# Kernel optimization log

Hardware: AMD Instinct MI355X
Metric: run time of the kernel (lower is better)

The kernel has to match this reference:

```python
import jax, jax.numpy as jnp
import numpy as np

N, D = 4096, 768
TEMPERATURE = 0.05


def setup_inputs() -> dict:
    key = jax.random.key(0)
    k1, k2 = jax.random.split(key)
    scale = 1.0 / jnp.sqrt(jnp.float32(D))  # keep dot/T in exp's safe range
    anchors = jax.random.normal(k1, (N, D), dtype=jnp.float32) * scale
    positives = jax.random.normal(k2, (N, D), dtype=jnp.float32) * scale
    return {"anchors": anchors, "positives": positives}


def reference(anchors, positives):
    # logits[j, i] = dot(anchor_j, positive_i) / T  -- single matmul replaces
    # the O(N^2) python-loop torch.dot calls.
    logits = jnp.einsum("jd,id->ji", anchors, positives) / TEMPERATURE  # [N, N]
    e = jnp.exp(logits)
    # Original code: negative_sum starts at exp(dot(anchor_j, positive_j)/T)
    # (the diagonal) and then adds exp(dot(anchor_j, positive_i)/T) for ALL i
    # (so the own positive is counted twice).
    denom = jnp.diagonal(e) + e.sum(axis=1)  # [N]
    # Original bug: positive_similarity is overwritten inside the inner loop,
    # so the numerator is the similarity to the LAST positive (index N-1).
    log_num = logits[:, -1]  # [N]
    loss = -(log_num - jnp.log(denom))
    return loss.sum()
```

## Files before the change

### kernel.cpp

```cpp
#include <hip/hip_runtime.h>
#include <hip/hip_bf16.h>

#define N 4096
#define D 768
#define LN2 0.69314718055994530942f
#define QSCALE 5.371583f

typedef __attribute__((ext_vector_type(4))) int   i32x4;
typedef __attribute__((ext_vector_type(8))) int   i32x8;
typedef __attribute__((ext_vector_type(4))) float f32x4;

#define EXP2F(x) __builtin_amdgcn_exp2f(x)
#define LOG2F(x) __builtin_amdgcn_logf(x)

#define GLDS16(g, l) __builtin_amdgcn_global_load_lds( \
    (const __attribute__((address_space(1))) void*)(g), \
    (__attribute__((address_space(3))) void*)(l), 16, 0, 0)


__global__ void convert_kernel(const float* __restrict__ A, const float* __restrict__ B,
                               unsigned* __restrict__ Af8, unsigned* __restrict__ Bf8,
                               float* __restrict__ out) {
    if (blockIdx.x == 0 && threadIdx.x == 0) out[0] = 0.0f;
    const int total = N * D / 4;
    int idx = blockIdx.x * blockDim.x + threadIdx.x;
    int stride = gridDim.x * blockDim.x;
    for (int i = idx; i < total; i += stride) {
        float4 a = ((const float4*)A)[i];
        float4 b = ((const float4*)B)[i];
        int pa = __builtin_amdgcn_cvt_pk_fp8_f32(a.x * QSCALE, a.y * QSCALE, 0, 0);
        pa     = __builtin_amdgcn_cvt_pk_fp8_f32(a.z * QSCALE, a.w * QSCALE, pa, 1);
        int pb = __builtin_amdgcn_cvt_pk_fp8_f32(b.x * QSCALE, b.y * QSCALE, 0, 0);
        pb     = __builtin_amdgcn_cvt_pk_fp8_f32(b.z * QSCALE, b.w * QSCALE, pb, 1);
        Af8[i] = (unsigned)pa;
        Bf8[i] = (unsigned)pb;
    }
}

__global__ __launch_bounds__(256) void gemm_kernel(const unsigned char* __restrict__ Af8,
                                                   const unsigned char* __restrict__ Bf8,
                                                   float* __restrict__ partial,
                                                   float* __restrict__ diagS,
                                                   float* __restrict__ lastS) {
    __shared__ __align__(16) unsigned char As[128 * 128];
    __shared__ __align__(16) unsigned char Bs[128 * 128];
    __shared__ float rowsum2[2][128];

    const int t    = threadIdx.x;
    const int bid  = blockIdx.x;
    const int xcd  = bid & 7;
    const int ii   = bid >> 3;
    const int bRow = ((xcd >> 1) << 3) + (ii >> 4);
    const int bCol = ((xcd & 1) << 4) + (ii & 15);
    const int lane = t & 63;
    const int w    = t >> 6;
    const int wr   = w >> 1;
    const int wc   = w & 1;
    const int lr   = lane & 15;
    const int hi   = lane >> 4;

    const int srow = t >> 3;
    const int sc   = t & 7;
    const int gcv  = sc ^ (srow & 7);
    const size_t aOff = (size_t)(bRow * 128 + srow) * D + gcv * 16;
    const size_t bOff = (size_t)(bCol * 128 + srow) * D + gcv * 16;

    f32x4 acc[4][4] = {};
    const int NT = D / 128;

    union Frag { i32x8 v; i32x4 h[2]; };

#define LDFRAG(DST, ARRBUF, ROW) do {                                                   \
    (DST).h[0] = *(const i32x4*)&(ARRBUF)[(ROW) * 128 + ((hi ^ (lr & 7)) * 16)];        \
    (DST).h[1] = *(const i32x4*)&(ARRBUF)[(ROW) * 128 + (((hi + 4) ^ (lr & 7)) * 16)];  \
} while (0)

    for (int tt = 0; tt < NT; ++tt) {
        const size_t kb = (size_t)tt * 128;
        #pragma unroll
        for (int inst = 0; inst < 4; ++inst) {
            GLDS16(Af8 + aOff + (size_t)inst * 32 * D + kb, &As[inst * 4096 + w * 1024]);
            GLDS16(Bf8 + bOff + (size_t)inst * 32 * D + kb, &Bs[inst * 4096 + w * 1024]);
        }
        asm volatile("s_waitcnt vmcnt(0)" ::: "memory");
        __builtin_amdgcn_s_barrier();
        __builtin_amdgcn_sched_barrier(0);

        Frag bfr[4];
        #pragma unroll
        for (int nf = 0; nf < 4; ++nf)
            LDFRAG(bfr[nf], Bs, wc * 64 + nf * 16 + lr);
        __builtin_amdgcn_s_setprio(1);
        #pragma unroll
        for (int mf = 0; mf < 4; ++mf) {
            Frag a8;
            LDFRAG(a8, As, wr * 64 + mf * 16 + lr);
            #pragma unroll
            for (int nf = 0; nf < 4; ++nf)
                acc[mf][nf] = __builtin_amdgcn_mfma_scale_f32_16x16x128_f8f6f4(
                    a8.v, bfr[nf].v, acc[mf][nf], 0, 0, 0, 0x7F7F7F7F, 0, 0x7F7F7F7F);
        }
        __builtin_amdgcn_s_setprio(0);
        asm volatile("s_waitcnt lgkmcnt(0)" ::: "memory");
        __builtin_amdgcn_sched_barrier(0);
        __builtin_amdgcn_s_barrier();
        __builtin_amdgcn_sched_barrier(0);
    }
#undef LDFRAG

    const int rifb = hi * 4;

    if (bRow == bCol && wr == wc) {
        #pragma unroll
        for (int mf = 0; mf < 4; ++mf)
            #pragma unroll
            for (int reg = 0; reg < 4; ++reg)
                if (lr == rifb + reg)
                    diagS[bRow * 128 + wr * 64 + mf * 16 + rifb + reg] = acc[mf][mf][reg];
    }

    if (bCol == (N / 128 - 1) && wc == 1 && lr == 15) {
        #pragma unroll
        for (int mf = 0; mf < 4; ++mf)
            #pragma unroll
            for (int reg = 0; reg < 4; ++reg)
                lastS[bRow * 128 + wr * 64 + mf * 16 + rifb + reg] = acc[mf][3][reg];
    }

    #pragma unroll
    for (int mf = 0; mf < 4; ++mf) {
        #pragma unroll
        for (int reg = 0; reg < 4; ++reg) {
            float s = EXP2F(acc[mf][0][reg]) + EXP2F(acc[mf][1][reg]) +
                      EXP2F(acc[mf][2][reg]) + EXP2F(acc[mf][3][reg]);
            s += __shfl_xor(s, 1);
            s += __shfl_xor(s, 2);
            s += __shfl_xor(s, 4);
            s += __shfl_xor(s, 8);
            if (lr == 0) rowsum2[wc][wr * 64 + mf * 16 + rifb + reg] = s;
        }
    }
    __syncthreads();
    if (t < 128) partial[(size_t)bCol * N + bRow * 128 + t] = rowsum2[0][t] + rowsum2[1][t];
}

__global__ void rowloss_kernel(const float* __restrict__ partial, const float* __restrict__ diagS,
                               const float* __restrict__ lastS, float* __restrict__ out) {
    const int j = blockIdx.x * 128 + threadIdx.x;
    float rs = 0.0f;
    #pragma unroll
    for (int tI = 0; tI < 32; ++tI) rs += partial[(size_t)tI * N + j];
    float denom = rs + EXP2F(diagS[j]);
    float lossj = LN2 * (LOG2F(denom) - lastS[j]);
    #pragma unroll
    for (int off = 1; off < 64; off <<= 1) lossj += __shfl_xor(lossj, off);
    __shared__ float ws2[2];
    if ((threadIdx.x & 63) == 0) ws2[threadIdx.x >> 6] = lossj;
    __syncthreads();
    if (threadIdx.x == 0) atomicAdd(out, ws2[0] + ws2[1]);
}

extern "C" void kernel_launch(void* const* d_in, const int* in_sizes, int n_in,
                              void* d_out, int out_size, void* d_ws, size_t ws_size,
                              hipStream_t stream) {
    const float* A = (const float*)d_in[0];
    const float* B = (const float*)d_in[1];
    float* out = (float*)d_out;
    char* ws = (char*)d_ws;

    unsigned char* Af8 = (unsigned char*)(ws);
    unsigned char* Bf8 = (unsigned char*)(ws + 3145728);
    float* partial     = (float*)(ws + 6291456);
    float* diagS       = (float*)(ws + 6815744);
    float* lastS       = (float*)(ws + 6832128);

    convert_kernel<<<1024, 256, 0, stream>>>(A, B, (unsigned*)Af8, (unsigned*)Bf8, out);
    gemm_kernel<<<1024, 256, 0, stream>>>(Af8, Bf8, partial, diagS, lastS);
    rowloss_kernel<<<32, 128, 0, stream>>>(partial, diagS, lastS, out);
}
```

Before: 34.21 us.

## Split GEMM load wait to overlap A fetch with B fragment reads; atomically reduce row sums

The K-loop now issues the B-tile loads before the A-tile loads and waits only for B (vmcnt(4)) before reading B fragments from LDS, then waits for A behind a second barrier. This lets the LDS reads of B overlap the remaining A global loads. Separately, per-tile row sums are accumulated with global atomicAdd into a zeroed N-length buffer instead of a 32xN partial array, which drops a shared-memory stage and barrier and shrinks the final reduction. The cost is an extra barrier per iteration, atomic contention (32 column tiles and 2 wave columns per row), and summation order that is no longer deterministic.

```diff
diff --git a/kernel.cpp b/kernel.cpp
--- a/kernel.cpp
+++ b/kernel.cpp
@@ -20,12 +20,13 @@
 
 __global__ void convert_kernel(const float* __restrict__ A, const float* __restrict__ B,
                                unsigned* __restrict__ Af8, unsigned* __restrict__ Bf8,
-                               float* __restrict__ out) {
-    if (blockIdx.x == 0 && threadIdx.x == 0) out[0] = 0.0f;
+                               float* __restrict__ partial, float* __restrict__ out) {
+    const int gtid = blockIdx.x * blockDim.x + threadIdx.x;
+    if (gtid == 0) out[0] = 0.0f;
+    if (gtid < N) partial[gtid] = 0.0f;
     const int total = N * D / 4;
-    int idx = blockIdx.x * blockDim.x + threadIdx.x;
-    int stride = gridDim.x * blockDim.x;
-    for (int i = idx; i < total; i += stride) {
+    const int stride = gridDim.x * blockDim.x;
+    for (int i = gtid; i < total; i += stride) {
         float4 a = ((const float4*)A)[i];
         float4 b = ((const float4*)B)[i];
         int pa = __builtin_amdgcn_cvt_pk_fp8_f32(a.x * QSCALE, a.y * QSCALE, 0, 0);
@@ -44,7 +45,6 @@
                                                    float* __restrict__ lastS) {
     __shared__ __align__(16) unsigned char As[128 * 128];
     __shared__ __align__(16) unsigned char Bs[128 * 128];
-    __shared__ float rowsum2[2][128];
 
     const int t    = threadIdx.x;
     const int bid  = blockIdx.x;
@@ -78,11 +78,13 @@
     for (int tt = 0; tt < NT; ++tt) {
         const size_t kb = (size_t)tt * 128;
         #pragma unroll
-        for (int inst = 0; inst < 4; ++inst) {
+        for (int inst = 0; inst < 4; ++inst)
+            GLDS16(Bf8 + bOff + (size_t)inst * 32 * D + kb, &Bs[inst * 4096 + w * 1024]);
+        #pragma unroll
+        for (int inst = 0; inst < 4; ++inst)
             GLDS16(Af8 + aOff + (size_t)inst * 32 * D + kb, &As[inst * 4096 + w * 1024]);
-            GLDS16(Bf8 + bOff + (size_t)inst * 32 * D + kb, &Bs[inst * 4096 + w * 1024]);
-        }
-        asm volatile("s_waitcnt vmcnt(0)" ::: "memory");
+
+        asm volatile("s_waitcnt vmcnt(4)" ::: "memory");
         __builtin_amdgcn_s_barrier();
         __builtin_amdgcn_sched_barrier(0);
 
@@ -90,6 +92,12 @@
         #pragma unroll
         for (int nf = 0; nf < 4; ++nf)
             LDFRAG(bfr[nf], Bs, wc * 64 + nf * 16 + lr);
+
+        asm volatile("s_waitcnt vmcnt(0)" ::: "memory");
+        __builtin_amdgcn_sched_barrier(0);
+        __builtin_amdgcn_s_barrier();
+        __builtin_amdgcn_sched_barrier(0);
+
         __builtin_amdgcn_s_setprio(1);
         #pragma unroll
         for (int mf = 0; mf < 4; ++mf) {
@@ -137,20 +145,16 @@
             s += __shfl_xor(s, 2);
             s += __shfl_xor(s, 4);
             s += __shfl_xor(s, 8);
-            if (lr == 0) rowsum2[wc][wr * 64 + mf * 16 + rifb + reg] = s;
+            if (lr == 0)
+                atomicAdd(&partial[bRow * 128 + wr * 64 + mf * 16 + rifb + reg], s);
         }
     }
-    __syncthreads();
-    if (t < 128) partial[(size_t)bCol * N + bRow * 128 + t] = rowsum2[0][t] + rowsum2[1][t];
 }
 
 __global__ void rowloss_kernel(const float* __restrict__ partial, const float* __restrict__ diagS,
                                const float* __restrict__ lastS, float* __restrict__ out) {
     const int j = blockIdx.x * 128 + threadIdx.x;
-    float rs = 0.0f;
-    #pragma unroll
-    for (int tI = 0; tI < 32; ++tI) rs += partial[(size_t)tI * N + j];
-    float denom = rs + EXP2F(diagS[j]);
+    float denom = partial[j] + EXP2F(diagS[j]);
     float lossj = LN2 * (LOG2F(denom) - lastS[j]);
     #pragma unroll
     for (int off = 1; off < 64; off <<= 1) lossj += __shfl_xor(lossj, off);
@@ -171,10 +175,10 @@
     unsigned char* Af8 = (unsigned char*)(ws);
     unsigned char* Bf8 = (unsigned char*)(ws + 3145728);
     float* partial     = (float*)(ws + 6291456);
-    float* diagS       = (float*)(ws + 6815744);
-    float* lastS       = (float*)(ws + 6832128);
+    float* diagS       = (float*)(ws + 6307840);
+    float* lastS       = (float*)(ws + 6324224);
 
-    convert_kernel<<<1024, 256, 0, stream>>>(A, B, (unsigned*)Af8, (unsigned*)Bf8, out);
+    convert_kernel<<<1024, 256, 0, stream>>>(A, B, (unsigned*)Af8, (unsigned*)Bf8, partial, out);
     gemm_kernel<<<1024, 256, 0, stream>>>(Af8, Bf8, partial, diagS, lastS);
     rowloss_kernel<<<32, 128, 0, stream>>>(partial, diagS, lastS, out);
 }
```

Measured after the change: 41.73 us. 1.22x slower.
